# Performance work log

Hardware: AMD Instinct MI355X
Metric: run time of the kernel (lower is better)

Reference implementation:

```python
import jax, jax.numpy as jnp
import numpy as np

NUM_TOKENS = 16384
HIDDEN = 4096
NUM_EXPERTS = 256
TOP_K = 8
N_GROUP = 8
TOPK_GROUP = 4
NORM_TOPK_PROB = True
ROUTED_SCALING_FACTOR = 1.0


def setup_inputs() -> dict:
    key = jax.random.key(0)
    k1, k2, k3 = jax.random.split(key, 3)
    hidden_states = jax.random.normal(k1, (NUM_TOKENS, HIDDEN), dtype=jnp.float32)
    weight = jax.random.normal(k2, (NUM_EXPERTS, HIDDEN), dtype=jnp.float32) * (HIDDEN ** -0.5)
    e_score_correction_bias = jax.random.normal(k3, (NUM_EXPERTS,), dtype=jnp.float32) * 0.01
    return {"hidden_states": hidden_states, "weight": weight,
            "e_score_correction_bias": e_score_correction_bias}


def reference(hidden_states, weight, e_score_correction_bias):
    num_tokens = hidden_states.shape[0]
    # router logits: [T, E]
    logits = jnp.einsum('th,eh->te', hidden_states.astype(jnp.float32),
                        weight.astype(jnp.float32))
    scores = jax.nn.sigmoid(logits)
    scores_for_choice = scores + e_score_correction_bias[None, :]
    # group scores: sum of top-2 within each group, [T, G]
    per_group = scores_for_choice.reshape(num_tokens, N_GROUP, NUM_EXPERTS // N_GROUP)
    top2_vals, _ = jax.lax.top_k(per_group, 2)
    group_scores = top2_vals.sum(axis=-1)
    # select topk_group groups, build mask over experts
    _, group_idx = jax.lax.top_k(group_scores, TOPK_GROUP)  # [T, topk_group]
    group_mask = jnp.zeros_like(group_scores).at[
        jnp.arange(num_tokens)[:, None], group_idx].set(1.0)  # [T, G]
    score_mask = jnp.repeat(group_mask, NUM_EXPERTS // N_GROUP, axis=1)  # [T, E]
    tmp_scores = jnp.where(score_mask > 0, scores_for_choice, -jnp.inf)
    # final top-k experts over masked scores
    _, topk_idx = jax.lax.top_k(tmp_scores, TOP_K)  # [T, K]
    topk_weight = jnp.take_along_axis(scores, topk_idx, axis=1)
    if TOP_K > 1 and NORM_TOPK_PROB:
        denom = topk_weight.sum(axis=-1, keepdims=True) + 1e-20
        topk_weight = topk_weight / denom
    topk_weight = topk_weight * ROUTED_SCALING_FACTOR
    return logits, topk_weight, topk_idx
```

## Files before the change

kernel.cpp:

```cpp
#include <hip/hip_runtime.h>
#include <hip/hip_bf16.h>
#include <math.h>

#define TKN 16384
#define HID 4096
#define NE  256
#define TOPK 8
#define NGRP 8
#define TOPG 4

#define BM 128
#define BN 128
#define BK 64
#define NKT (HID / BK)

#define ASTR 144
#define APL  (BM * ASTR)
#define BPL  (BN * 128)
#define BIMG (2 * BPL)

typedef _Float16 half8 __attribute__((ext_vector_type(8)));
typedef float    f32x4 __attribute__((ext_vector_type(4)));

static __device__ __forceinline__ unsigned pkrtz(float x, float y) {
    auto r = __builtin_amdgcn_cvt_pkrtz(x, y);
    return __builtin_bit_cast(unsigned, r);
}
static __device__ __forceinline__ float hi_mask(float a) {
    return __uint_as_float(__float_as_uint(a) & 0xFFFFE000u);
}

__global__ __launch_bounds__(256) void prep_b(const float* __restrict__ B,
                                              unsigned char* __restrict__ ws)
{
    const int gid = blockIdx.x * 256 + threadIdx.x;
    const int e   = gid >> 9;
    const int k0  = (gid & 511) * 8;
    const float* src = B + (size_t)e * HID + k0;
    float v[8];
    #pragma unroll
    for (int i = 0; i < 8; ++i) v[i] = src[i];
    unsigned hw[4], lw[4];
    #pragma unroll
    for (int j = 0; j < 4; ++j) {
        const float x0 = v[2*j], x1 = v[2*j+1];
        const float h0 = hi_mask(x0), h1 = hi_mask(x1);
        hw[j] = pkrtz(h0, h1);
        lw[j] = pkrtz(x0 - h0, x1 - h1);
    }
    const int cb  = e >> 7;
    const int row = e & 127;
    const int kt  = k0 >> 6;
    const int x   = ((k0 & 63) * 2) ^ ((row & 7) << 4);
    unsigned char* img = ws + (size_t)(cb * NKT + kt) * BIMG + row * 128 + x;
    *(uint4*)(img)       = make_uint4(hw[0], hw[1], hw[2], hw[3]);
    *(uint4*)(img + BPL) = make_uint4(lw[0], lw[1], lw[2], lw[3]);
}

__global__ __launch_bounds__(1024, 4) void gemm_mfma(
    const float* __restrict__ A, const unsigned char* __restrict__ Bws,
    float* __restrict__ C)
{
    __shared__ __align__(16) unsigned char sA[2][2][APL];
    __shared__ __align__(16) unsigned char sB[2][BIMG];

    const int tid  = threadIdx.x;
    const int lane = tid & 63;
    const int wave = tid >> 6;
    const int wg = wave >> 3;
    const int wr = (wave >> 2) & 1;
    const int wc = wave & 3;

    const int bid  = blockIdx.x;
    const int mb   = (bid & 7) * 16 + (bid >> 4);
    const int cb   = (bid >> 3) & 1;
    const int row0 = mb * BM;

    const int arow = tid >> 4;
    const int acol = (tid & 15) * 4;
    const float* aG0 = A + (size_t)(row0 + arow) * HID + acol;
    const float* aG1 = aG0 + (size_t)64 * HID;
    const int aw0 = arow * ASTR + acol * 2;
    const int aw1 = (arow + 64) * ASTR + acol * 2;

    const unsigned char* bG = Bws + (size_t)cb * NKT * BIMG + tid * 16;
    const int bw0 = tid * 16, bw1 = 16384 + tid * 16;

    const int afr = wr * 64 + (lane & 15);
    const int afo = afr * ASTR + (wg * 4 + (lane >> 4)) * 16;
    const int bfr = wc * 32 + (lane & 15);
    const int bfx = (wg * 4 + (lane >> 4)) * 16;

    f32x4 acc[4][2];
    #pragma unroll
    for (int i = 0; i < 4; ++i) { acc[i][0] = (f32x4)0.f; acc[i][1] = (f32x4)0.f; }

    float4 av0, av1; uint4 bv0, bv1;

    av0 = *(const float4*)(aG0);
    av1 = *(const float4*)(aG1);
    bv0 = *(const uint4*)(bG);
    bv1 = *(const uint4*)(bG + 16384);
    {
        const float h0 = hi_mask(av0.x), h1 = hi_mask(av0.y),
                    h2 = hi_mask(av0.z), h3 = hi_mask(av0.w);
        *(uint2*)&sA[0][0][aw0] = make_uint2(pkrtz(h0, h1), pkrtz(h2, h3));
        *(uint2*)&sA[0][1][aw0] = make_uint2(pkrtz(av0.x - h0, av0.y - h1),
                                             pkrtz(av0.z - h2, av0.w - h3));
        const float g0 = hi_mask(av1.x), g1 = hi_mask(av1.y),
                    g2 = hi_mask(av1.z), g3 = hi_mask(av1.w);
        *(uint2*)&sA[0][0][aw1] = make_uint2(pkrtz(g0, g1), pkrtz(g2, g3));
        *(uint2*)&sA[0][1][aw1] = make_uint2(pkrtz(av1.x - g0, av1.y - g1),
                                             pkrtz(av1.z - g2, av1.w - g3));
        *(uint4*)&sB[0][bw0] = bv0;
        *(uint4*)&sB[0][bw1] = bv1;
    }
    __syncthreads();

    for (int kt = 0; kt < NKT; ++kt) {
        const int cur = kt & 1;
        const bool more = (kt + 1 < NKT);
        if (more) {
            av0 = *(const float4*)(aG0 + (kt + 1) * BK);
            av1 = *(const float4*)(aG1 + (kt + 1) * BK);
            const unsigned char* bp = bG + (size_t)(kt + 1) * BIMG;
            bv0 = *(const uint4*)(bp);
            bv1 = *(const uint4*)(bp + 16384);
        }
        {
            half8 bf[2][2];
            #pragma unroll
            for (int nt = 0; nt < 2; ++nt) {
                const int r  = bfr + nt * 16;
                const int ad = r * 128 + (bfx ^ ((r & 7) << 4));
                bf[nt][0] = *(const half8*)&sB[cur][ad];
                bf[nt][1] = *(const half8*)&sB[cur][BPL + ad];
            }
            #pragma unroll
            for (int mt = 0; mt < 4; ++mt) {
                const int ad = afo + mt * 16 * ASTR;
                const half8 ah = *(const half8*)&sA[cur][0][ad];
                const half8 al = *(const half8*)&sA[cur][1][ad];
                #pragma unroll
                for (int nt = 0; nt < 2; ++nt) {
                    f32x4 c = acc[mt][nt];
                    c = __builtin_amdgcn_mfma_f32_16x16x32_f16(ah, bf[nt][0], c, 0, 0, 0);
                    c = __builtin_amdgcn_mfma_f32_16x16x32_f16(ah, bf[nt][1], c, 0, 0, 0);
                    c = __builtin_amdgcn_mfma_f32_16x16x32_f16(al, bf[nt][0], c, 0, 0, 0);
                    acc[mt][nt] = c;
                }
            }
        }
        if (more) {
            const int nb = cur ^ 1;
            const float h0 = hi_mask(av0.x), h1 = hi_mask(av0.y),
                        h2 = hi_mask(av0.z), h3 = hi_mask(av0.w);
            *(uint2*)&sA[nb][0][aw0] = make_uint2(pkrtz(h0, h1), pkrtz(h2, h3));
            *(uint2*)&sA[nb][1][aw0] = make_uint2(pkrtz(av0.x - h0, av0.y - h1),
                                                  pkrtz(av0.z - h2, av0.w - h3));
            const float g0 = hi_mask(av1.x), g1 = hi_mask(av1.y),
                        g2 = hi_mask(av1.z), g3 = hi_mask(av1.w);
            *(uint2*)&sA[nb][0][aw1] = make_uint2(pkrtz(g0, g1), pkrtz(g2, g3));
            *(uint2*)&sA[nb][1][aw1] = make_uint2(pkrtz(av1.x - g0, av1.y - g1),
                                                  pkrtz(av1.z - g2, av1.w - g3));
            *(uint4*)&sB[nb][bw0] = bv0;
            *(uint4*)&sB[nb][bw1] = bv1;
        }
        __syncthreads();
    }

    unsigned char* red = &sA[0][0][0];
    const int fbase = (wave & 7) * 8192;
    if (wg == 1) {
        #pragma unroll
        for (int mt = 0; mt < 4; ++mt)
            #pragma unroll
            for (int nt = 0; nt < 2; ++nt)
                *(f32x4*)&red[fbase + (mt * 2 + nt) * 1024 + lane * 16] = acc[mt][nt];
    }
    __syncthreads();
    if (wg == 0) {
        #pragma unroll
        for (int mt = 0; mt < 4; ++mt) {
            #pragma unroll
            for (int nt = 0; nt < 2; ++nt) {
                f32x4 o = acc[mt][nt] +
                          *(const f32x4*)&red[fbase + (mt * 2 + nt) * 1024 + lane * 16];
                const int r0 = row0 + wr * 64 + mt * 16 + (lane >> 4) * 4;
                const int cc = cb * 128 + wc * 32 + nt * 16 + (lane & 15);
                #pragma unroll
                for (int r = 0; r < 4; ++r)
                    C[(size_t)(r0 + r) * NE + cc] = o[r];
            }
        }
    }
}

__global__ __launch_bounds__(256) void router_topk_kernel(
    const float* __restrict__ logits, const float* __restrict__ bias,
    float* __restrict__ out_w, float* __restrict__ out_i)
{
    const int wid  = threadIdx.x >> 6;
    const int lane = threadIdx.x & 63;
    const int token = blockIdx.x * 4 + wid;

    const float* row = logits + (size_t)token * NE;
    const float4 lg = *(const float4*)&row[lane * 4];

    float sig[4], sc[4];
    {
        const float l4[4] = {lg.x, lg.y, lg.z, lg.w};
        #pragma unroll
        for (int j = 0; j < 4; ++j) {
            sig[j] = 1.f / (1.f + expf(-l4[j]));
            sc[j]  = sig[j] + bias[lane * 4 + j];
        }
    }

    float m1 = sc[0], m2 = -INFINITY;
    #pragma unroll
    for (int j = 1; j < 4; ++j) {
        if (sc[j] > m1) { m2 = m1; m1 = sc[j]; }
        else if (sc[j] > m2) { m2 = sc[j]; }
    }
    #pragma unroll
    for (int off = 1; off < 8; off <<= 1) {
        const float o1 = __shfl_xor(m1, off);
        const float o2 = __shfl_xor(m2, off);
        const float lo = fminf(m1, o1);
        m1 = fmaxf(m1, o1);
        m2 = fmaxf(lo, fmaxf(m2, o2));
    }
    const float gscore = m1 + m2;

    const int gmy = lane >> 3;
    int rank = 0;
    #pragma unroll
    for (int g = 0; g < NGRP; ++g) {
        const float gs = __shfl(gscore, g * 8);
        if (gs > gscore || (gs == gscore && g < gmy)) ++rank;
    }
    if (rank >= TOPG) {
        #pragma unroll
        for (int j = 0; j < 4; ++j) sc[j] = -INFINITY;
    }

    float wk[TOPK]; int ik[TOPK];
    float wsum = 0.f;
    #pragma unroll
    for (int k = 0; k < TOPK; ++k) {
        float bv = sc[0]; int bi = lane * 4;
        #pragma unroll
        for (int j = 1; j < 4; ++j)
            if (sc[j] > bv) { bv = sc[j]; bi = lane * 4 + j; }
        #pragma unroll
        for (int off = 1; off < 64; off <<= 1) {
            const float v2 = __shfl_xor(bv, off);
            const int   i2 = __shfl_xor(bi, off);
            if (v2 > bv || (v2 == bv && i2 < bi)) { bv = v2; bi = i2; }
        }
        const int owner = bi >> 2;
        const int j = bi & 3;
        const float sv = (j == 0) ? sig[0] : (j == 1) ? sig[1] : (j == 2) ? sig[2] : sig[3];
        const float w = __shfl(sv, owner);
        wk[k] = w; ik[k] = bi; wsum += w;
        if (lane == owner) {
            if (j == 0) sc[0] = -INFINITY;
            else if (j == 1) sc[1] = -INFINITY;
            else if (j == 2) sc[2] = -INFINITY;
            else sc[3] = -INFINITY;
        }
    }

    if (lane == 0) {
        const float denom = wsum + 1e-20f;
        #pragma unroll
        for (int k = 0; k < TOPK; ++k) {
            out_w[(size_t)token * TOPK + k] = wk[k] / denom;
            out_i[(size_t)token * TOPK + k] = (float)ik[k];
        }
    }
}

extern "C" void kernel_launch(void* const* d_in, const int* in_sizes, int n_in,
                              void* d_out, int out_size, void* d_ws, size_t ws_size,
                              hipStream_t stream) {
    const float* hidden = (const float*)d_in[0];
    const float* weight = (const float*)d_in[1];
    const float* bias   = (const float*)d_in[2];

    float* logits = (float*)d_out;
    float* out_w  = logits + (size_t)TKN * NE;
    float* out_i  = out_w + (size_t)TKN * TOPK;

    unsigned char* bpl = (unsigned char*)d_ws;

    prep_b<<<512, 256, 0, stream>>>(weight, bpl);
    gemm_mfma<<<256, 1024, 0, stream>>>(hidden, bpl, logits);
    router_topk_kernel<<<TKN / 4, 256, 0, stream>>>(logits, bias, out_w, out_i);
}
```

Baseline: 150.1 us.

## Load pre-split B fragments directly from global and swizzle A tile in LDS

The GEMM kernel stops staging the pre-converted B image through shared memory. Each wave now reads its hi/lo half8 B fragments straight from global memory (L2-resident) every k-step, and only the A tile is double-buffered in LDS, now with an XOR swizzle instead of row padding and wider 16-byte stores. This cuts LDS footprint and store traffic and may improve occupancy, at the cost of uncoalesced per-wave global B loads that sit on the critical path ahead of the MFMAs, with a sched_barrier fencing them.

```diff
diff --git a/kernel.cpp b/kernel.cpp
--- a/kernel.cpp
+++ b/kernel.cpp
@@ -10,14 +10,9 @@
 #define TOPG 4
 
 #define BM 128
-#define BN 128
 #define BK 64
 #define NKT (HID / BK)
-
-#define ASTR 144
-#define APL  (BM * ASTR)
-#define BPL  (BN * 128)
-#define BIMG (2 * BPL)
+#define BIMG 32768
 
 typedef _Float16 half8 __attribute__((ext_vector_type(8)));
 typedef float    f32x4 __attribute__((ext_vector_type(4)));
@@ -53,16 +48,15 @@
     const int kt  = k0 >> 6;
     const int x   = ((k0 & 63) * 2) ^ ((row & 7) << 4);
     unsigned char* img = ws + (size_t)(cb * NKT + kt) * BIMG + row * 128 + x;
-    *(uint4*)(img)       = make_uint4(hw[0], hw[1], hw[2], hw[3]);
-    *(uint4*)(img + BPL) = make_uint4(lw[0], lw[1], lw[2], lw[3]);
+    *(uint4*)(img)         = make_uint4(hw[0], hw[1], hw[2], hw[3]);
+    *(uint4*)(img + 16384) = make_uint4(lw[0], lw[1], lw[2], lw[3]);
 }
 
 __global__ __launch_bounds__(1024, 4) void gemm_mfma(
     const float* __restrict__ A, const unsigned char* __restrict__ Bws,
     float* __restrict__ C)
 {
-    __shared__ __align__(16) unsigned char sA[2][2][APL];
-    __shared__ __align__(16) unsigned char sB[2][BIMG];
+    __shared__ __align__(16) unsigned char smem[2][2][16384];
 
     const int tid  = threadIdx.x;
     const int lane = tid & 63;
@@ -76,107 +70,94 @@
     const int cb   = (bid >> 3) & 1;
     const int row0 = mb * BM;
 
-    const int arow = tid >> 4;
-    const int acol = (tid & 15) * 4;
-    const float* aG0 = A + (size_t)(row0 + arow) * HID + acol;
-    const float* aG1 = aG0 + (size_t)64 * HID;
-    const int aw0 = arow * ASTR + acol * 2;
-    const int aw1 = (arow + 64) * ASTR + acol * 2;
-
-    const unsigned char* bG = Bws + (size_t)cb * NKT * BIMG + tid * 16;
-    const int bw0 = tid * 16, bw1 = 16384 + tid * 16;
-
-    const int afr = wr * 64 + (lane & 15);
-    const int afo = afr * ASTR + (wg * 4 + (lane >> 4)) * 16;
-    const int bfr = wc * 32 + (lane & 15);
-    const int bfx = (wg * 4 + (lane >> 4)) * 16;
+    const int arow = tid >> 3;
+    const int aseg = (tid & 7) * 8;
+    const float* aG = A + (size_t)(row0 + arow) * HID + aseg;
+    const int awx = arow * 128 + ((aseg * 2) ^ ((arow & 7) << 4));
+
+    const int kx    = ((wg * 64) + ((lane >> 4) << 4)) ^ ((lane & 7) << 4);
+    const int aRowB = (wr * 64 + (lane & 15)) * 128;
+    const unsigned char* bBase = Bws + (size_t)cb * NKT * BIMG;
+    const int boff0 = (wc * 32 + (lane & 15)) * 128 + kx;
+    const int boff1 = boff0 + 16 * 128;
 
     f32x4 acc[4][2];
     #pragma unroll
     for (int i = 0; i < 4; ++i) { acc[i][0] = (f32x4)0.f; acc[i][1] = (f32x4)0.f; }
 
-    float4 av0, av1; uint4 bv0, bv1;
-
-    av0 = *(const float4*)(aG0);
-    av1 = *(const float4*)(aG1);
-    bv0 = *(const uint4*)(bG);
-    bv1 = *(const uint4*)(bG + 16384);
+    float4 v0, v1;
+
+    v0 = *(const float4*)(aG);
+    v1 = *(const float4*)(aG + 4);
     {
-        const float h0 = hi_mask(av0.x), h1 = hi_mask(av0.y),
-                    h2 = hi_mask(av0.z), h3 = hi_mask(av0.w);
-        *(uint2*)&sA[0][0][aw0] = make_uint2(pkrtz(h0, h1), pkrtz(h2, h3));
-        *(uint2*)&sA[0][1][aw0] = make_uint2(pkrtz(av0.x - h0, av0.y - h1),
-                                             pkrtz(av0.z - h2, av0.w - h3));
-        const float g0 = hi_mask(av1.x), g1 = hi_mask(av1.y),
-                    g2 = hi_mask(av1.z), g3 = hi_mask(av1.w);
-        *(uint2*)&sA[0][0][aw1] = make_uint2(pkrtz(g0, g1), pkrtz(g2, g3));
-        *(uint2*)&sA[0][1][aw1] = make_uint2(pkrtz(av1.x - g0, av1.y - g1),
-                                             pkrtz(av1.z - g2, av1.w - g3));
-        *(uint4*)&sB[0][bw0] = bv0;
-        *(uint4*)&sB[0][bw1] = bv1;
+        const float h0 = hi_mask(v0.x), h1 = hi_mask(v0.y),
+                    h2 = hi_mask(v0.z), h3 = hi_mask(v0.w);
+        const float h4 = hi_mask(v1.x), h5 = hi_mask(v1.y),
+                    h6 = hi_mask(v1.z), h7 = hi_mask(v1.w);
+        *(uint4*)&smem[0][0][awx] = make_uint4(pkrtz(h0, h1), pkrtz(h2, h3),
+                                               pkrtz(h4, h5), pkrtz(h6, h7));
+        *(uint4*)&smem[0][1][awx] = make_uint4(pkrtz(v0.x - h0, v0.y - h1),
+                                               pkrtz(v0.z - h2, v0.w - h3),
+                                               pkrtz(v1.x - h4, v1.y - h5),
+                                               pkrtz(v1.z - h6, v1.w - h7));
     }
     __syncthreads();
 
     for (int kt = 0; kt < NKT; ++kt) {
-        const int cur = kt & 1;
-        const bool more = (kt + 1 < NKT);
+        const unsigned char* ub = &smem[kt & 1][0][0];
+        const bool more = (kt != NKT - 1);
+
         if (more) {
-            av0 = *(const float4*)(aG0 + (kt + 1) * BK);
-            av1 = *(const float4*)(aG1 + (kt + 1) * BK);
-            const unsigned char* bp = bG + (size_t)(kt + 1) * BIMG;
-            bv0 = *(const uint4*)(bp);
-            bv1 = *(const uint4*)(bp + 16384);
-        }
-        {
-            half8 bf[2][2];
-            #pragma unroll
-            for (int nt = 0; nt < 2; ++nt) {
-                const int r  = bfr + nt * 16;
-                const int ad = r * 128 + (bfx ^ ((r & 7) << 4));
-                bf[nt][0] = *(const half8*)&sB[cur][ad];
-                bf[nt][1] = *(const half8*)&sB[cur][BPL + ad];
-            }
-            #pragma unroll
-            for (int mt = 0; mt < 4; ++mt) {
-                const int ad = afo + mt * 16 * ASTR;
-                const half8 ah = *(const half8*)&sA[cur][0][ad];
-                const half8 al = *(const half8*)&sA[cur][1][ad];
-                #pragma unroll
-                for (int nt = 0; nt < 2; ++nt) {
-                    f32x4 c = acc[mt][nt];
-                    c = __builtin_amdgcn_mfma_f32_16x16x32_f16(ah, bf[nt][0], c, 0, 0, 0);
-                    c = __builtin_amdgcn_mfma_f32_16x16x32_f16(ah, bf[nt][1], c, 0, 0, 0);
-                    c = __builtin_amdgcn_mfma_f32_16x16x32_f16(al, bf[nt][0], c, 0, 0, 0);
-                    acc[mt][nt] = c;
-                }
-            }
-        }
+            v0 = *(const float4*)(aG + (kt + 1) * BK);
+            v1 = *(const float4*)(aG + (kt + 1) * BK + 4);
+        }
+        const unsigned char* bp = bBase + (size_t)kt * BIMG;
+        const half8 bh0 = *(const half8*)(bp + boff0);
+        const half8 bl0 = *(const half8*)(bp + 16384 + boff0);
+        const half8 bh1 = *(const half8*)(bp + boff1);
+        const half8 bl1 = *(const half8*)(bp + 16384 + boff1);
+        __builtin_amdgcn_sched_barrier(0);
+
+        #pragma unroll
+        for (int mt = 0; mt < 4; ++mt) {
+            const half8 ah = *(const half8*)(ub + aRowB + mt * 2048 + kx);
+            const half8 al = *(const half8*)(ub + 16384 + aRowB + mt * 2048 + kx);
+            f32x4 c0 = acc[mt][0];
+            c0 = __builtin_amdgcn_mfma_f32_16x16x32_f16(ah, bh0, c0, 0, 0, 0);
+            c0 = __builtin_amdgcn_mfma_f32_16x16x32_f16(ah, bl0, c0, 0, 0, 0);
+            c0 = __builtin_amdgcn_mfma_f32_16x16x32_f16(al, bh0, c0, 0, 0, 0);
+            acc[mt][0] = c0;
+            f32x4 c1 = acc[mt][1];
+            c1 = __builtin_amdgcn_mfma_f32_16x16x32_f16(ah, bh1, c1, 0, 0, 0);
+            c1 = __builtin_amdgcn_mfma_f32_16x16x32_f16(ah, bl1, c1, 0, 0, 0);
+            c1 = __builtin_amdgcn_mfma_f32_16x16x32_f16(al, bh1, c1, 0, 0, 0);
+            acc[mt][1] = c1;
+        }
+
         if (more) {
-            const int nb = cur ^ 1;
-            const float h0 = hi_mask(av0.x), h1 = hi_mask(av0.y),
-                        h2 = hi_mask(av0.z), h3 = hi_mask(av0.w);
-            *(uint2*)&sA[nb][0][aw0] = make_uint2(pkrtz(h0, h1), pkrtz(h2, h3));
-            *(uint2*)&sA[nb][1][aw0] = make_uint2(pkrtz(av0.x - h0, av0.y - h1),
-                                                  pkrtz(av0.z - h2, av0.w - h3));
-            const float g0 = hi_mask(av1.x), g1 = hi_mask(av1.y),
-                        g2 = hi_mask(av1.z), g3 = hi_mask(av1.w);
-            *(uint2*)&sA[nb][0][aw1] = make_uint2(pkrtz(g0, g1), pkrtz(g2, g3));
-            *(uint2*)&sA[nb][1][aw1] = make_uint2(pkrtz(av1.x - g0, av1.y - g1),
-                                                  pkrtz(av1.z - g2, av1.w - g3));
-            *(uint4*)&sB[nb][bw0] = bv0;
-            *(uint4*)&sB[nb][bw1] = bv1;
+            const int nb = (kt + 1) & 1;
+            const float h0 = hi_mask(v0.x), h1 = hi_mask(v0.y),
+                        h2 = hi_mask(v0.z), h3 = hi_mask(v0.w);
+            const float h4 = hi_mask(v1.x), h5 = hi_mask(v1.y),
+                        h6 = hi_mask(v1.z), h7 = hi_mask(v1.w);
+            *(uint4*)&smem[nb][0][awx] = make_uint4(pkrtz(h0, h1), pkrtz(h2, h3),
+                                                    pkrtz(h4, h5), pkrtz(h6, h7));
+            *(uint4*)&smem[nb][1][awx] = make_uint4(pkrtz(v0.x - h0, v0.y - h1),
+                                                    pkrtz(v0.z - h2, v0.w - h3),
+                                                    pkrtz(v1.x - h4, v1.y - h5),
+                                                    pkrtz(v1.z - h6, v1.w - h7));
         }
         __syncthreads();
     }
 
-    unsigned char* red = &sA[0][0][0];
-    const int fbase = (wave & 7) * 8192;
+    float* redf = (float*)&smem[0][0][0];
+    const int fb = (wave & 7) * 2048 + lane * 4;
     if (wg == 1) {
         #pragma unroll
         for (int mt = 0; mt < 4; ++mt)
             #pragma unroll
             for (int nt = 0; nt < 2; ++nt)
-                *(f32x4*)&red[fbase + (mt * 2 + nt) * 1024 + lane * 16] = acc[mt][nt];
+                *(f32x4*)&redf[fb + (mt * 2 + nt) * 256] = acc[mt][nt];
     }
     __syncthreads();
     if (wg == 0) {
@@ -184,8 +165,7 @@
         for (int mt = 0; mt < 4; ++mt) {
             #pragma unroll
             for (int nt = 0; nt < 2; ++nt) {
-                f32x4 o = acc[mt][nt] +
-                          *(const f32x4*)&red[fbase + (mt * 2 + nt) * 1024 + lane * 16];
+                f32x4 o = acc[mt][nt] + *(const f32x4*)&redf[fb + (mt * 2 + nt) * 256];
                 const int r0 = row0 + wr * 64 + mt * 16 + (lane >> 4) * 4;
                 const int cc = cb * 128 + wc * 32 + nt * 16 + (lane & 15);
                 #pragma unroll
```

Result: slower. 189.2 us (+26.1%).
